# Kernel tuning notes

Measured on AMD Instinct MI355X. Metric: run time of the kernel, lower is better.

The kernel has to match this reference:

```python
import jax, jax.numpy as jnp
import numpy as np

B, S, D, V = 32, 1024, 768, 32000


def setup_inputs() -> dict:
    key = jax.random.key(0)
    ks = jax.random.split(key, 12)
    scale = 0.02
    return {
        "tokens": jax.random.randint(ks[0], (B, S), 0, V, dtype=jnp.int32),
        "mask": jax.random.randint(ks[1], (B, S), 0, 2, dtype=jnp.int32),
        "emb": jax.random.normal(ks[2], (V, D), dtype=jnp.float32) * scale,
        "wq": jax.random.normal(ks[3], (D, D), dtype=jnp.float32) * scale,
        "wk": jax.random.normal(ks[4], (D, D), dtype=jnp.float32) * scale,
        "wv": jax.random.normal(ks[5], (D, D), dtype=jnp.float32) * scale,
        "ln_g": jnp.ones((D,), dtype=jnp.float32),
        "ln_b": jnp.zeros((D,), dtype=jnp.float32),
        "w1": jax.random.normal(ks[6], (D, D), dtype=jnp.float32) * scale,
        "b1": jnp.zeros((D,), dtype=jnp.float32),
        "wh": jax.random.normal(ks[7], (D, 2), dtype=jnp.float32) * scale,
        "bh": jnp.zeros((2,), dtype=jnp.float32),
    }


def reference(tokens, mask, emb, wq, wk, wv, ln_g, ln_b, w1, b1, wh, bh):
    # embedding lookup: [B,S,D]
    x = emb[tokens]
    q = x @ wq
    k = x @ wk
    v = x @ wv
    # unscaled attention scores: [B,S,S]
    s = jnp.einsum("bsd,btd->bst", q, k)
    # additive padding mask (mask==1 -> -1e9), broadcast over query dim
    s = s + (-1e9) * mask.astype(s.dtype)[:, None, :]
    a = jax.nn.softmax(s, axis=-1)
    o = jnp.einsum("bst,btd->bsd", a, v)
    # classify on first token
    cls = o[:, 0, :]  # [B,D]
    mu = jnp.mean(cls, axis=-1, keepdims=True)
    var = jnp.var(cls, axis=-1, keepdims=True)
    h = (cls - mu) * jax.lax.rsqrt(var + 1e-5) * ln_g + ln_b
    h = jax.nn.gelu(h @ w1 + b1, approximate=False)
    logits = h @ wh + bh  # [B,2]
    return (logits, a)
```

## Files before the change

### kernel.cpp

```cpp
#include <hip/hip_runtime.h>
#include <hip/hip_bf16.h>

#define NB 32
#define SS 1024
#define DD 768

typedef __attribute__((ext_vector_type(8))) short bf16x8;
typedef __attribute__((ext_vector_type(4))) float f32x4;

__device__ inline ushort f2bf(float f) {
    union { float f; unsigned u; } x;
    x.f = f;
    unsigned r = (x.u + 0x7fffu + ((x.u >> 16) & 1u)) >> 16;
    return (ushort)r;
}

__device__ inline float bf2f(ushort u) {
    union { unsigned u; float f; } x;
    x.u = ((unsigned)u) << 16;
    return x.f;
}

#define GLOBAL_PTR(x) ((const __attribute__((address_space(1))) void*)(x))
#define LDS_PTR(x)    ((__attribute__((address_space(3))) void*)(x))

__global__ void k_prep(const int* __restrict__ tokens, const float* __restrict__ emb,
                       const float* __restrict__ wq, const float* __restrict__ wk,
                       ushort* __restrict__ xb, ushort* __restrict__ wqb, ushort* __restrict__ wkb) {
    const int bid = blockIdx.x;
    if (bid < 24576) {
        int i = (bid * 256 + threadIdx.x) * 4;
        int row = i / DD;
        int col = i - row * DD;
        int tok = tokens[row];
        const float4 v = *(const float4*)(emb + (size_t)tok * DD + col);
        ushort4 o;
        o.x = f2bf(v.x); o.y = f2bf(v.y); o.z = f2bf(v.z); o.w = f2bf(v.w);
        *(ushort4*)(xb + (size_t)row * DD + col) = o;
    } else {
        const int b2 = bid - 24576;
        const float* src = (b2 < 576) ? wq : wk;
        ushort* dst = (b2 < 576) ? wqb : wkb;
        const int local = (b2 < 576) ? b2 : b2 - 576;
        const int i = (local * 256 + threadIdx.x) * 4;
        const float4 v = *(const float4*)(src + i);
        ushort4 o;
        o.x = f2bf(v.x); o.y = f2bf(v.y); o.z = f2bf(v.z); o.w = f2bf(v.w);
        *(ushort4*)(dst + i) = o;
    }
}

__global__ __launch_bounds__(256, 2) void k_gemm_s(const ushort* __restrict__ A,
                                                   const ushort* __restrict__ Bt,
                                                   ushort* __restrict__ Cb) {
    constexpr int BK = 64;
    __shared__ ushort As[2][128 * BK];
    __shared__ ushort Bs[2][128 * BK];
    const int tid = threadIdx.x;
    const int wave = tid >> 6, lane = tid & 63;
    const int bx = blockIdx.x, by = blockIdx.y;
    const size_t abase = (size_t)bx * 128 * DD;
    const size_t bbase = (size_t)by * 128 * DD;
    const int r = tid >> 3;
    const int cc = (tid & 7) * 8;

    auto stage = [&](int buf, int k0) {
#pragma unroll
        for (int i = 0; i < 4; i++) {
            __builtin_amdgcn_global_load_lds(GLOBAL_PTR(A + abase + (size_t)(r + i * 32) * DD + k0 + cc),
                                             LDS_PTR(&As[buf][(r + i * 32) * BK + cc]), 16, 0, 0);
            __builtin_amdgcn_global_load_lds(GLOBAL_PTR(Bt + bbase + (size_t)(r + i * 32) * DD + k0 + cc),
                                             LDS_PTR(&Bs[buf][(r + i * 32) * BK + cc]), 16, 0, 0);
        }
    };

    f32x4 acc[4][4] = {};
    const int wm = (wave >> 1) * 64, wn = (wave & 1) * 64;
    const int lr = lane & 15, lc = (lane >> 4) * 8;

    stage(0, 0);
    __syncthreads();
    int cur = 0;
#pragma unroll 1
    for (int k0 = 0; k0 < DD; k0 += BK) {
        if (k0 + BK < DD) stage(cur ^ 1, k0 + BK);
        const ushort* as = As[cur];
        const ushort* bs = Bs[cur];
#pragma unroll
        for (int kk = 0; kk < 2; kk++) {
            bf16x8 af[4], bfv[4];
#pragma unroll
            for (int m = 0; m < 4; m++)
                af[m] = *(const bf16x8*)(as + (wm + m * 16 + lr) * BK + kk * 32 + lc);
#pragma unroll
            for (int n = 0; n < 4; n++)
                bfv[n] = *(const bf16x8*)(bs + (wn + n * 16 + lr) * BK + kk * 32 + lc);
#pragma unroll
            for (int m = 0; m < 4; m++)
#pragma unroll
                for (int n = 0; n < 4; n++)
                    acc[m][n] = __builtin_amdgcn_mfma_f32_16x16x32_bf16(af[m], bfv[n], acc[m][n], 0, 0, 0);
        }
        __syncthreads();
        cur ^= 1;
    }
    const int rowbase = bx * 128 + wm + (lane >> 4) * 4;
    const int colbase = by * 128 + wn + (lane & 15);
#pragma unroll
    for (int m = 0; m < 4; m++)
#pragma unroll
        for (int n = 0; n < 4; n++)
#pragma unroll
            for (int j = 0; j < 4; j++)
                Cb[(size_t)(rowbase + m * 16 + j) * DD + colbase + n * 16] = f2bf(acc[m][n][j]);
}

#define HALF_USH (128 * 64)
__global__ __launch_bounds__(512, 2) void k_gemm256b(const ushort* __restrict__ A,
                                                     const ushort* __restrict__ Bt,
                                                     ushort* __restrict__ Cu) {
    __shared__ ushort As[2][2][HALF_USH];
    __shared__ ushort Bs[2][2][HALF_USH];
    const int tid = threadIdx.x;
    const int wid = tid >> 6, lane = tid & 63;
    const int wm = wid >> 2, wn = wid & 3;
    const int la = lane & 15;

    const int wgid = blockIdx.x;
    const int g = wgid >> 7, w = wgid & 127;
    const int b = g * 8 + (w & 7);
    const int tile = w >> 3;
    const int bx = tile & 3, by = tile >> 2;
    const ushort* Ag = A + (size_t)b * SS * DD + (size_t)bx * 256 * DD;
    const ushort* Bg = Bt + (size_t)b * SS * DD + (size_t)by * 256 * DD;
    Cu += (size_t)b * SS * 2048;

    int s_r[2], s_c[2], s_d[2];
#pragma unroll
    for (int l = 0; l < 2; l++) {
        const int L = (l * 512 + tid) * 16;
        const int r = L >> 7;
        const int cb = L & 127;
        s_r[l] = r;
        s_c[l] = (cb ^ ((r & 7) << 4)) >> 1;
        s_d[l] = L >> 1;
    }

    auto stage_half = [&](ushort* dst, const ushort* gsrc) {
#pragma unroll
        for (int l = 0; l < 2; l++)
            __builtin_amdgcn_global_load_lds(GLOBAL_PTR(gsrc + (size_t)s_r[l] * DD + s_c[l]),
                                             LDS_PTR(dst + s_d[l]), 16, 0, 0);
    };

    const int swz = (la & 7) << 4;
    const int off_k0 = (((lane >> 4) << 4) ^ swz) >> 1;
    const int off_k1 = ((64 | ((lane >> 4) << 4)) ^ swz) >> 1;

    f32x4 acc[8][4] = {};

    stage_half(&As[0][0][0], Ag);
    stage_half(&As[0][1][0], Ag + (size_t)128 * DD);
    stage_half(&Bs[0][0][0], Bg);
    stage_half(&Bs[0][1][0], Bg + (size_t)128 * DD);
    __syncthreads();

#pragma unroll 1
    for (int t = 0; t < 12; t++) {
        const int buf = t & 1;
        const ushort* Ah = &As[buf][wm][0];
        const ushort* Bh = &Bs[buf][wn >> 1][0];
        const int brow0 = (wn & 1) * 64;
        const int kt = (t + 1) * 64;
        bf16x8 bfv[4][2];
#pragma unroll
        for (int q = 0; q < 4; q++) {
            if (q == 0) {
#pragma unroll
                for (int n = 0; n < 4; n++) {
                    const int rr = brow0 + n * 16 + la;
                    bfv[n][0] = *(const bf16x8*)(Bh + rr * 64 + off_k0);
                    bfv[n][1] = *(const bf16x8*)(Bh + rr * 64 + off_k1);
                }
                if (t < 11) {
                    stage_half(&As[buf ^ 1][0][0], Ag + kt);
                    stage_half(&As[buf ^ 1][1][0], Ag + (size_t)128 * DD + kt);
                    stage_half(&Bs[buf ^ 1][0][0], Bg + kt);
                    stage_half(&Bs[buf ^ 1][1][0], Bg + (size_t)128 * DD + kt);
                }
            }
            bf16x8 af[2][2];
#pragma unroll
            for (int dm = 0; dm < 2; dm++) {
                const int rr = (q * 2 + dm) * 16 + la;
                af[dm][0] = *(const bf16x8*)(Ah + rr * 64 + off_k0);
                af[dm][1] = *(const bf16x8*)(Ah + rr * 64 + off_k1);
            }
            __builtin_amdgcn_s_setprio(1);
#pragma unroll
            for (int dm = 0; dm < 2; dm++)
#pragma unroll
                for (int n = 0; n < 4; n++)
#pragma unroll
                    for (int kk = 0; kk < 2; kk++)
                        acc[q * 2 + dm][n] = __builtin_amdgcn_mfma_f32_16x16x32_bf16(
                            af[dm][kk], bfv[n][kk], acc[q * 2 + dm][n], 0, 0, 0);
            __builtin_amdgcn_s_setprio(0);
            if (q < 3) __builtin_amdgcn_s_barrier();
        }
        __syncthreads();
    }

    const int rowbase = bx * 256 + wm * 128 + (lane >> 4) * 4;
    const int colbase = by * 256 + wn * 64 + la;
#pragma unroll
    for (int m = 0; m < 8; m++)
#pragma unroll
        for (int n = 0; n < 4; n++)
#pragma unroll
            for (int j = 0; j < 4; j++)
                Cu[(size_t)(rowbase + m * 16 + j) * 2048 + colbase + n * 16] = f2bf(acc[m][n][j]);
}

__global__ __launch_bounds__(256) void k_smax(const ushort* __restrict__ su, const int* __restrict__ mask,
                                              float* __restrict__ a) {
    const int tid = threadIdx.x, lane = tid & 63;
    const int row = blockIdx.x * 4 + (tid >> 6);
    const int b = row >> 10;
    const int* mrow = mask + b * SS;
    const ushort* srow = su + (size_t)row * 2048;

    float e[4][4];
    float psum = 0.f;
#pragma unroll
    for (int g = 0; g < 4; g++) {
        const int t = g * 256 + lane * 4;
        const int4 mk = *(const int4*)(mrow + t);
        const ushort4 sv4 = *(const ushort4*)(srow + t);
        e[g][0] = __expf(bf2f(sv4.x) + (mk.x ? -1e9f : 0.0f));
        e[g][1] = __expf(bf2f(sv4.y) + (mk.y ? -1e9f : 0.0f));
        e[g][2] = __expf(bf2f(sv4.z) + (mk.z ? -1e9f : 0.0f));
        e[g][3] = __expf(bf2f(sv4.w) + (mk.w ? -1e9f : 0.0f));
        psum += e[g][0] + e[g][1] + e[g][2] + e[g][3];
    }
#pragma unroll
    for (int off = 32; off; off >>= 1) psum += __shfl_xor(psum, off);
    const float inv = 1.0f / psum;
    float* arow = a + (size_t)row * SS;
#pragma unroll
    for (int g = 0; g < 4; g++) {
        const int t = g * 256 + lane * 4;
        float4 o;
        o.x = e[g][0] * inv; o.y = e[g][1] * inv; o.z = e[g][2] * inv; o.w = e[g][3] * inv;
        *(float4*)(arow + t) = o;
    }
}

__global__ __launch_bounds__(256) void k_xbar(const float* __restrict__ a, const int* __restrict__ tokens,
                                              const float* __restrict__ emb, float* __restrict__ part) {
    const int b = blockIdx.x >> 3, c = blockIdx.x & 7;
    __shared__ float a0s[128];
    __shared__ int toks[128];
    const int tid = threadIdx.x;
    if (tid < 128) {
        a0s[tid] = a[(size_t)b * SS * SS + c * 128 + tid];
        toks[tid] = tokens[b * SS + c * 128 + tid];
    }
    __syncthreads();
    float acc0 = 0.f, acc1 = 0.f, acc2 = 0.f;
#pragma unroll 4
    for (int t = 0; t < 128; t++) {
        const float at = a0s[t];
        const float* er = emb + (size_t)toks[t] * DD;
        acc0 = fmaf(at, er[tid], acc0);
        acc1 = fmaf(at, er[tid + 256], acc1);
        acc2 = fmaf(at, er[tid + 512], acc2);
    }
    float* p = part + ((size_t)c * NB + b) * DD;
    p[tid] = acc0; p[tid + 256] = acc1; p[tid + 512] = acc2;
}

__global__ __launch_bounds__(128) void k_cls(const float* __restrict__ part, const float* __restrict__ wv,
                                             float* __restrict__ cls) {
    const int b = blockIdx.y, tid = threadIdx.x;
    const int c = blockIdx.x * 128 + tid;
    __shared__ float xb[DD];
#pragma unroll
    for (int j = 0; j < 6; j++) {
        const int k = tid + j * 128;
        float s = 0.f;
#pragma unroll
        for (int p = 0; p < 8; p++) s += part[((size_t)p * NB + b) * DD + k];
        xb[k] = s;
    }
    __syncthreads();
    float acc = 0.f;
#pragma unroll 8
    for (int k = 0; k < DD; k++) acc = fmaf(xb[k], wv[(size_t)k * DD + c], acc);
    cls[(size_t)b * DD + c] = acc;
}

__global__ __launch_bounds__(128) void k_mlp(const float* __restrict__ cls, const float* __restrict__ ln_g,
                                             const float* __restrict__ ln_b, const float* __restrict__ w1,
                                             const float* __restrict__ b1, const float* __restrict__ wh,
                                             float* __restrict__ part_l) {
    const int b = blockIdx.y, tid = threadIdx.x;
    __shared__ float h[DD];
    __shared__ float red2[2];
    float v[6];
#pragma unroll
    for (int q = 0; q < 6; q++) v[q] = cls[(size_t)b * DD + tid + q * 128];
    float s = v[0] + v[1] + v[2] + v[3] + v[4] + v[5];
#pragma unroll
    for (int off = 32; off; off >>= 1) s += __shfl_xor(s, off);
    if ((tid & 63) == 0) red2[tid >> 6] = s;
    __syncthreads();
    const float mu = (red2[0] + red2[1]) * (1.0f / DD);
    float dv = 0.f;
#pragma unroll
    for (int q = 0; q < 6; q++) { const float d = v[q] - mu; dv += d * d; }
#pragma unroll
    for (int off = 32; off; off >>= 1) dv += __shfl_xor(dv, off);
    __syncthreads();
    if ((tid & 63) == 0) red2[tid >> 6] = dv;
    __syncthreads();
    const float var = (red2[0] + red2[1]) * (1.0f / DD);
    const float sc = 1.0f / sqrtf(var + 1e-5f);
#pragma unroll
    for (int q = 0; q < 6; q++) {
        const int d = tid + q * 128;
        h[d] = (v[q] - mu) * sc * ln_g[d] + ln_b[d];
    }
    __syncthreads();

    const int j = blockIdx.x * 128 + tid;
    float p = b1[j];
#pragma unroll 8
    for (int d = 0; d < DD; d++) p = fmaf(h[d], w1[(size_t)d * DD + j], p);
    const float g = 0.5f * p * (1.0f + erff(p * 0.70710678118654752f));
    float l0 = g * wh[j * 2 + 0];
    float l1 = g * wh[j * 2 + 1];
#pragma unroll
    for (int off = 32; off; off >>= 1) { l0 += __shfl_xor(l0, off); l1 += __shfl_xor(l1, off); }
    __shared__ float r0[2], r1[2];
    if ((tid & 63) == 0) { r0[tid >> 6] = l0; r1[tid >> 6] = l1; }
    __syncthreads();
    if (tid == 0) {
        part_l[((size_t)b * 6 + blockIdx.x) * 2 + 0] = r0[0] + r0[1];
        part_l[((size_t)b * 6 + blockIdx.x) * 2 + 1] = r1[0] + r1[1];
    }
}

__global__ __launch_bounds__(64) void k_final(const float* __restrict__ part_l, const float* __restrict__ bh,
                                              float* __restrict__ out) {
    const int b = threadIdx.x;
    if (b < NB) {
        float l0 = bh[0], l1 = bh[1];
#pragma unroll
        for (int c = 0; c < 6; c++) {
            l0 += part_l[((size_t)b * 6 + c) * 2 + 0];
            l1 += part_l[((size_t)b * 6 + c) * 2 + 1];
        }
        out[b * 2 + 0] = l0;
        out[b * 2 + 1] = l1;
    }
}

extern "C" void kernel_launch(void* const* d_in, const int* in_sizes, int n_in,
                              void* d_out, int out_size, void* d_ws, size_t ws_size,
                              hipStream_t stream) {
    const int*   tokens = (const int*)d_in[0];
    const int*   mask   = (const int*)d_in[1];
    const float* emb    = (const float*)d_in[2];
    const float* wq     = (const float*)d_in[3];
    const float* wk     = (const float*)d_in[4];
    const float* wv     = (const float*)d_in[5];
    const float* ln_g   = (const float*)d_in[6];
    const float* ln_b   = (const float*)d_in[7];
    const float* w1     = (const float*)d_in[8];
    const float* b1     = (const float*)d_in[9];
    const float* wh     = (const float*)d_in[10];
    const float* bh     = (const float*)d_in[11];
    float* out = (float*)d_out;

    char* ws = (char*)d_ws;
    const size_t XB = (size_t)NB * SS * DD * 2;
    const size_t WB = (size_t)DD * DD * 2;
    ushort* xb  = (ushort*)ws;
    ushort* yb  = (ushort*)(ws + XB);
    ushort* wqb = (ushort*)(ws + 2 * XB);
    ushort* wkb = (ushort*)(ws + 2 * XB + WB);
    ushort* Wt  = (ushort*)(ws + 2 * XB + 2 * WB);
    char*   p4  = ws + 2 * XB + 3 * WB;
    float*  part   = (float*)p4;
    float*  cls    = (float*)(p4 + 786432);
    float*  part_l = (float*)(p4 + 786432 + 98304);

    float* a_region = out + 64;

    k_prep<<<24576 + 1152, 256, 0, stream>>>(tokens, emb, wq, wk, xb, wqb, wkb);
    k_gemm_s<<<dim3(6, 6), 256, 0, stream>>>(wkb, wqb, Wt);
    k_gemm_s<<<dim3(256, 6), 256, 0, stream>>>(xb, Wt, yb);
    k_gemm256b<<<512, 512, 0, stream>>>(yb, xb, (ushort*)a_region);
    k_smax<<<8192, 256, 0, stream>>>((const ushort*)a_region, mask, a_region);
    k_xbar<<<256, 256, 0, stream>>>(a_region, tokens, emb, part);
    k_cls<<<dim3(6, NB), 128, 0, stream>>>(part, wv, cls);
    k_mlp<<<dim3(6, NB), 128, 0, stream>>>(cls, ln_g, ln_b, w1, b1, wh, part_l);
    k_final<<<1, 64, 0, stream>>>(part_l, bh, out);
}
```

Before: 326.4 us.

## Triple-buffer QK^T GEMM with K=32 stages and single barrier per step

```diff
diff --git a/kernel.cpp b/kernel.cpp
--- a/kernel.cpp
+++ b/kernel.cpp
@@ -115,16 +115,16 @@
                 Cb[(size_t)(rowbase + m * 16 + j) * DD + colbase + n * 16] = f2bf(acc[m][n][j]);
 }
 
-#define HALF_USH (128 * 64)
-__global__ __launch_bounds__(512, 2) void k_gemm256b(const ushort* __restrict__ A,
-                                                     const ushort* __restrict__ Bt,
-                                                     ushort* __restrict__ Cu) {
-    __shared__ ushort As[2][2][HALF_USH];
-    __shared__ ushort Bs[2][2][HALF_USH];
+#define NT 24
+__global__ __launch_bounds__(512) void k_gemm256b(const ushort* __restrict__ A,
+                                                  const ushort* __restrict__ Bt,
+                                                  ushort* __restrict__ Cu) {
+    __shared__ ushort Ab[3][256 * 32];
+    __shared__ ushort Bb[3][256 * 32];
     const int tid = threadIdx.x;
     const int wid = tid >> 6, lane = tid & 63;
     const int wm = wid >> 2, wn = wid & 3;
-    const int la = lane & 15;
+    const int la = lane & 15, lg = lane >> 4;
 
     const int wgid = blockIdx.x;
     const int g = wgid >> 7, w = wgid & 127;
@@ -135,80 +135,78 @@
     const ushort* Bg = Bt + (size_t)b * SS * DD + (size_t)by * 256 * DD;
     Cu += (size_t)b * SS * 2048;
 
-    int s_r[2], s_c[2], s_d[2];
+    int st_r[2], st_c[2], st_d[2];
 #pragma unroll
     for (int l = 0; l < 2; l++) {
-        const int L = (l * 512 + tid) * 16;
-        const int r = L >> 7;
-        const int cb = L & 127;
-        s_r[l] = r;
-        s_c[l] = (cb ^ ((r & 7) << 4)) >> 1;
-        s_d[l] = L >> 1;
-    }
-
-    auto stage_half = [&](ushort* dst, const ushort* gsrc) {
+        const int idx = l * 512 + tid;
+        const int r = idx >> 2;
+        const int c = idx & 3;
+        st_r[l] = r;
+        st_c[l] = (c ^ ((r >> 1) & 3)) << 3;
+        st_d[l] = idx * 8;
+    }
+
+    auto stage = [&](int bufi, int k0) {
 #pragma unroll
         for (int l = 0; l < 2; l++)
-            __builtin_amdgcn_global_load_lds(GLOBAL_PTR(gsrc + (size_t)s_r[l] * DD + s_c[l]),
-                                             LDS_PTR(dst + s_d[l]), 16, 0, 0);
+            __builtin_amdgcn_global_load_lds(GLOBAL_PTR(Ag + (size_t)st_r[l] * DD + k0 + st_c[l]),
+                                             LDS_PTR(&Ab[bufi][0] + st_d[l]), 16, 0, 0);
+#pragma unroll
+        for (int l = 0; l < 2; l++)
+            __builtin_amdgcn_global_load_lds(GLOBAL_PTR(Bg + (size_t)st_r[l] * DD + k0 + st_c[l]),
+                                             LDS_PTR(&Bb[bufi][0] + st_d[l]), 16, 0, 0);
     };
 
-    const int swz = (la & 7) << 4;
-    const int off_k0 = (((lane >> 4) << 4) ^ swz) >> 1;
-    const int off_k1 = ((64 | ((lane >> 4) << 4)) ^ swz) >> 1;
+    const int koff = (lg ^ ((la >> 1) & 3)) << 3;
 
     f32x4 acc[8][4] = {};
 
-    stage_half(&As[0][0][0], Ag);
-    stage_half(&As[0][1][0], Ag + (size_t)128 * DD);
-    stage_half(&Bs[0][0][0], Bg);
-    stage_half(&Bs[0][1][0], Bg + (size_t)128 * DD);
-    __syncthreads();
+    stage(0, 0);
+    stage(1, 32);
 
 #pragma unroll 1
-    for (int t = 0; t < 12; t++) {
-        const int buf = t & 1;
-        const ushort* Ah = &As[buf][wm][0];
-        const ushort* Bh = &Bs[buf][wn >> 1][0];
-        const int brow0 = (wn & 1) * 64;
-        const int kt = (t + 1) * 64;
-        bf16x8 bfv[4][2];
-#pragma unroll
-        for (int q = 0; q < 4; q++) {
-            if (q == 0) {
-#pragma unroll
-                for (int n = 0; n < 4; n++) {
-                    const int rr = brow0 + n * 16 + la;
-                    bfv[n][0] = *(const bf16x8*)(Bh + rr * 64 + off_k0);
-                    bfv[n][1] = *(const bf16x8*)(Bh + rr * 64 + off_k1);
-                }
-                if (t < 11) {
-                    stage_half(&As[buf ^ 1][0][0], Ag + kt);
-                    stage_half(&As[buf ^ 1][1][0], Ag + (size_t)128 * DD + kt);
-                    stage_half(&Bs[buf ^ 1][0][0], Bg + kt);
-                    stage_half(&Bs[buf ^ 1][1][0], Bg + (size_t)128 * DD + kt);
-                }
-            }
-            bf16x8 af[2][2];
-#pragma unroll
-            for (int dm = 0; dm < 2; dm++) {
-                const int rr = (q * 2 + dm) * 16 + la;
-                af[dm][0] = *(const bf16x8*)(Ah + rr * 64 + off_k0);
-                af[dm][1] = *(const bf16x8*)(Ah + rr * 64 + off_k1);
-            }
-            __builtin_amdgcn_s_setprio(1);
-#pragma unroll
-            for (int dm = 0; dm < 2; dm++)
-#pragma unroll
-                for (int n = 0; n < 4; n++)
-#pragma unroll
-                    for (int kk = 0; kk < 2; kk++)
-                        acc[q * 2 + dm][n] = __builtin_amdgcn_mfma_f32_16x16x32_bf16(
-                            af[dm][kk], bfv[n][kk], acc[q * 2 + dm][n], 0, 0, 0);
-            __builtin_amdgcn_s_setprio(0);
-            if (q < 3) __builtin_amdgcn_s_barrier();
-        }
-        __syncthreads();
+    for (int t = 0; t < NT - 1; ++t) {
+        asm volatile("s_waitcnt vmcnt(4)" ::: "memory");
+        __builtin_amdgcn_sched_barrier(0);
+        __builtin_amdgcn_s_barrier();
+        if (t + 2 < NT) stage((t + 2) % 3, (t + 2) * 32);
+        const ushort* ab = &Ab[t % 3][0];
+        const ushort* bb = &Bb[t % 3][0];
+        bf16x8 af[8], bfv[4];
+#pragma unroll
+        for (int m = 0; m < 8; m++)
+            af[m] = *(const bf16x8*)(ab + (wm * 128 + m * 16 + la) * 32 + koff);
+#pragma unroll
+        for (int n = 0; n < 4; n++)
+            bfv[n] = *(const bf16x8*)(bb + (wn * 64 + n * 16 + la) * 32 + koff);
+        __builtin_amdgcn_s_setprio(1);
+#pragma unroll
+        for (int m = 0; m < 8; m++)
+#pragma unroll
+            for (int n = 0; n < 4; n++)
+                acc[m][n] = __builtin_amdgcn_mfma_f32_16x16x32_bf16(af[m], bfv[n], acc[m][n], 0, 0, 0);
+        __builtin_amdgcn_s_setprio(0);
+    }
+    asm volatile("s_waitcnt vmcnt(0)" ::: "memory");
+    __builtin_amdgcn_sched_barrier(0);
+    __builtin_amdgcn_s_barrier();
+    {
+        const ushort* ab = &Ab[(NT - 1) % 3][0];
+        const ushort* bb = &Bb[(NT - 1) % 3][0];
+        bf16x8 af[8], bfv[4];
+#pragma unroll
+        for (int m = 0; m < 8; m++)
+            af[m] = *(const bf16x8*)(ab + (wm * 128 + m * 16 + la) * 32 + koff);
+#pragma unroll
+        for (int n = 0; n < 4; n++)
+            bfv[n] = *(const bf16x8*)(bb + (wn * 64 + n * 16 + la) * 32 + koff);
+        __builtin_amdgcn_s_setprio(1);
+#pragma unroll
+        for (int m = 0; m < 8; m++)
+#pragma unroll
+            for (int n = 0; n < 4; n++)
+                acc[m][n] = __builtin_amdgcn_mfma_f32_16x16x32_bf16(af[m], bfv[n], acc[m][n], 0, 0, 0);
+        __builtin_amdgcn_s_setprio(0);
     }
 
     const int rowbase = bx * 256 + wm * 128 + (lane >> 4) * 4;
```

Measured after the change: 339.0 us. 3.9% more time.
